# Kernel tuning notes

Measured on AMD Instinct MI355X. Metric: run time of the kernel, lower is better.

The kernel has to match this reference:

```python
import jax, jax.numpy as jnp
import numpy as np

BATCH = 65536
AR_ORDER = 16
U_DIM = 15
REGRESSOR_DIM = AR_ORDER + U_DIM + 1  # 32
SEQUENCE_LENGTH = 1024


def setup_inputs() -> dict:
    key = jax.random.key(0)
    k1, k2, k3 = jax.random.split(key, 3)
    y = jax.random.normal(k1, (BATCH, AR_ORDER), dtype=jnp.float32)
    u = jax.random.normal(k2, (BATCH, U_DIM), dtype=jnp.float32)
    w = jax.random.normal(k3, (REGRESSOR_DIM,), dtype=jnp.float32) * (1.0 / np.sqrt(REGRESSOR_DIM))
    return {"y": y, "u": u, "w": w}


def reference(y, u, w):
    ar = y.shape[1]  # ar_order
    w_ar = w[:ar]                 # weights on the AR window
    w_u = w[ar:-1]                # weights on exogenous input u
    w_b = w[-1]                   # weight on the appended ones column
    # u and the ones column are constant over time: precompute their contribution. [B]
    const = u @ w_u + w_b

    def step(window, _):
        pred = window @ w_ar + const                      # [B]
        new_window = jnp.concatenate([window[:, 1:], pred[:, None]], axis=1)
        return new_window, pred

    _, preds = jax.lax.scan(step, y, None, length=SEQUENCE_LENGTH - ar)  # [S-ar, B]
    return jnp.concatenate([y, preds.T], axis=1)  # [B, S]
```

## Files before the change

### kernel.cpp

```cpp
#include <hip/hip_runtime.h>

#define BATCH 65536
#define AR 16
#define UD 15
#define SEQ 1024

__global__ __launch_bounds__(64) void arx_kernel(
    const float* __restrict__ y,
    const float* __restrict__ u,
    const float* __restrict__ w,
    float* __restrict__ out)
{
    __shared__ float buf[64][33];

    const int lane = threadIdx.x;
    const int row0 = blockIdx.x * 64;
    const int row  = row0 + lane;

    float w_ar[AR];
#pragma unroll
    for (int k = 0; k < AR; ++k) w_ar[k] = w[k];

    float cst = w[AR + UD];
#pragma unroll
    for (int j = 0; j < UD; ++j) cst = fmaf(u[row * UD + j], w[AR + j], cst);

    float win[AR];
#pragma unroll
    for (int k = 0; k < AR; ++k) win[k] = y[row * AR + k];

    const int half = lane >> 5;
    const int c    = lane & 31;

#pragma unroll
    for (int k = 0; k < AR; ++k) buf[lane][k] = win[k];
#pragma unroll
    for (int j = 0; j < 16; ++j) {
        float p0 = cst, p1 = 0.0f;
#pragma unroll
        for (int k = 0; k < 8; ++k)  p0 = fmaf(win[(j + k) & 15], w_ar[k], p0);
#pragma unroll
        for (int k = 8; k < 16; ++k) p1 = fmaf(win[(j + k) & 15], w_ar[k], p1);
        float p = p0 + p1;
        win[j & 15] = p;
        buf[lane][16 + j] = p;
    }
    __syncthreads();
#pragma unroll
    for (int k = 0; k < 32; ++k) {
        out[(size_t)(row0 + 2 * k + half) * SEQ + c] = buf[2 * k + half][c];
    }
    __syncthreads();

    for (int cb = 1; cb < 32; ++cb) {
#pragma unroll
        for (int j = 0; j < 32; ++j) {
            float p0 = cst, p1 = 0.0f;
#pragma unroll
            for (int k = 0; k < 8; ++k)  p0 = fmaf(win[(j + k) & 15], w_ar[k], p0);
#pragma unroll
            for (int k = 8; k < 16; ++k) p1 = fmaf(win[(j + k) & 15], w_ar[k], p1);
            float p = p0 + p1;
            win[j & 15] = p;
            buf[lane][j] = p;
        }
        __syncthreads();
        const int tb = cb * 32;
#pragma unroll
        for (int k = 0; k < 32; ++k) {
            out[(size_t)(row0 + 2 * k + half) * SEQ + tb + c] = buf[2 * k + half][c];
        }
        __syncthreads();
    }
}

extern "C" void kernel_launch(void* const* d_in, const int* in_sizes, int n_in,
                              void* d_out, int out_size, void* d_ws, size_t ws_size,
                              hipStream_t stream) {
    const float* y = (const float*)d_in[0];
    const float* u = (const float*)d_in[1];
    const float* w = (const float*)d_in[2];
    float* out = (float*)d_out;

    arx_kernel<<<dim3(BATCH / 64), dim3(64), 0, stream>>>(y, u, w, out);
}
```

Baseline: 276.6 us.

## Replace sequential AR recurrence with precomputed impulse-response matrix GEMM

A tiny one-block kernel first unrolls the linear recurrence on basis vectors, producing a 1024x17 matrix G that maps each row's 16 initial values plus its constant term straight to every output timestep. The main kernel then computes each output as an independent 17-term dot product, and a new second grid dimension splits the sequence into chunks so more blocks run in parallel. This removes the serial time dependency in the main kernel, at the cost of a serial prologue kernel, reads of G from global memory, and rounding that differs from the step-by-step recurrence.

```diff
diff --git a/kernel.cpp b/kernel.cpp
--- a/kernel.cpp
+++ b/kernel.cpp
@@ -4,11 +4,47 @@
 #define AR 16
 #define UD 15
 #define SEQ 1024
+#define RDIM 17
+#define CPB 256
 
-__global__ __launch_bounds__(64) void arx_kernel(
+__global__ __launch_bounds__(64) void gamma_kernel(
+    const float* __restrict__ w, float* __restrict__ G)
+{
+    const int i = threadIdx.x;
+    float w_ar[AR];
+#pragma unroll
+    for (int k = 0; k < AR; ++k) w_ar[k] = w[k];
+
+    const float e16 = (i == 16) ? 1.0f : 0.0f;
+    float ring[AR];
+#pragma unroll
+    for (int k = 0; k < AR; ++k) ring[k] = (i == k) ? 1.0f : 0.0f;
+
+    if (i < RDIM) {
+#pragma unroll
+        for (int t = 0; t < AR; ++t) G[t * RDIM + i] = (i == t) ? 1.0f : 0.0f;
+    }
+
+    for (int tb = 0; tb < (SEQ - AR) / AR; ++tb) {
+#pragma unroll
+        for (int s = 0; s < AR; ++s) {
+            float p0 = e16, p1 = 0.0f;
+#pragma unroll
+            for (int k = 0; k < 8; ++k)  p0 = fmaf(ring[(s + k) & 15], w_ar[k], p0);
+#pragma unroll
+            for (int k = 8; k < 16; ++k) p1 = fmaf(ring[(s + k) & 15], w_ar[k], p1);
+            const float p = p0 + p1;
+            ring[s & 15] = p;
+            if (i < RDIM) G[(AR + tb * AR + s) * RDIM + i] = p;
+        }
+    }
+}
+
+__global__ __launch_bounds__(64) void arx_gemm_kernel(
     const float* __restrict__ y,
     const float* __restrict__ u,
     const float* __restrict__ w,
+    const float* __restrict__ G,
     float* __restrict__ out)
 {
     __shared__ float buf[64][33];
@@ -16,59 +52,35 @@
     const int lane = threadIdx.x;
     const int row0 = blockIdx.x * 64;
     const int row  = row0 + lane;
+    const int cbase = blockIdx.y * CPB;
 
-    float w_ar[AR];
+    float r[RDIM];
 #pragma unroll
-    for (int k = 0; k < AR; ++k) w_ar[k] = w[k];
-
-    float cst = w[AR + UD];
+    for (int k = 0; k < AR; ++k) r[k] = y[row * AR + k];
+    float c = w[AR + UD];
 #pragma unroll
-    for (int j = 0; j < UD; ++j) cst = fmaf(u[row * UD + j], w[AR + j], cst);
-
-    float win[AR];
-#pragma unroll
-    for (int k = 0; k < AR; ++k) win[k] = y[row * AR + k];
+    for (int j = 0; j < UD; ++j) c = fmaf(u[row * UD + j], w[AR + j], c);
+    r[16] = c;
 
     const int half = lane >> 5;
-    const int c    = lane & 31;
+    const int cc   = lane & 31;
 
-#pragma unroll
-    for (int k = 0; k < AR; ++k) buf[lane][k] = win[k];
-#pragma unroll
-    for (int j = 0; j < 16; ++j) {
-        float p0 = cst, p1 = 0.0f;
-#pragma unroll
-        for (int k = 0; k < 8; ++k)  p0 = fmaf(win[(j + k) & 15], w_ar[k], p0);
-#pragma unroll
-        for (int k = 8; k < 16; ++k) p1 = fmaf(win[(j + k) & 15], w_ar[k], p1);
-        float p = p0 + p1;
-        win[j & 15] = p;
-        buf[lane][16 + j] = p;
-    }
-    __syncthreads();
-#pragma unroll
-    for (int k = 0; k < 32; ++k) {
-        out[(size_t)(row0 + 2 * k + half) * SEQ + c] = buf[2 * k + half][c];
-    }
-    __syncthreads();
-
-    for (int cb = 1; cb < 32; ++cb) {
+    for (int ch = 0; ch < CPB / 32; ++ch) {
+        const int tb = cbase + ch * 32;
 #pragma unroll
         for (int j = 0; j < 32; ++j) {
-            float p0 = cst, p1 = 0.0f;
+            const int t = tb + j;
+            float a0 = 0.0f, a1 = 0.0f;
 #pragma unroll
-            for (int k = 0; k < 8; ++k)  p0 = fmaf(win[(j + k) & 15], w_ar[k], p0);
+            for (int i = 0; i < 8; ++i)      a0 = fmaf(r[i], G[t * RDIM + i], a0);
 #pragma unroll
-            for (int k = 8; k < 16; ++k) p1 = fmaf(win[(j + k) & 15], w_ar[k], p1);
-            float p = p0 + p1;
-            win[j & 15] = p;
-            buf[lane][j] = p;
+            for (int i = 8; i < RDIM; ++i)   a1 = fmaf(r[i], G[t * RDIM + i], a1);
+            buf[lane][j] = a0 + a1;
         }
         __syncthreads();
-        const int tb = cb * 32;
 #pragma unroll
         for (int k = 0; k < 32; ++k) {
-            out[(size_t)(row0 + 2 * k + half) * SEQ + tb + c] = buf[2 * k + half][c];
+            out[(size_t)(row0 + 2 * k + half) * SEQ + tb + cc] = buf[2 * k + half][cc];
         }
         __syncthreads();
     }
@@ -81,6 +93,8 @@
     const float* u = (const float*)d_in[1];
     const float* w = (const float*)d_in[2];
     float* out = (float*)d_out;
+    float* G   = (float*)d_ws;
 
-    arx_kernel<<<dim3(BATCH / 64), dim3(64), 0, stream>>>(y, u, w, out);
+    gamma_kernel<<<dim3(1), dim3(64), 0, stream>>>(w, G);
+    arx_gemm_kernel<<<dim3(BATCH / 64, SEQ / CPB), dim3(64), 0, stream>>>(y, u, w, G, out);
 }
```

New measurement: 332.6 us. +20.2%, slower.
